# Kernel optimization log

Measured on AMD Instinct MI355X. Metric: run time of the kernel, lower is better.

The kernel has to match this reference:

```python
import jax, jax.numpy as jnp
import numpy as np

# irreps = 128x0e + 64x1e + 32x2e  (dim = 128 + 64*3 + 32*5 = 480)
# hidden = 512x0e + 256x1e + 128x2e ; gate scalars = (256+128) x0e
N = 65536
M0, M1, M2 = 128, 64, 32          # input multiplicities per degree l=0,1,2
H0, H1, H2 = 512, 256, 128        # hidden multiplicities
G = H1 + H2                       # number of sigmoid gate scalars
EPS = 1e-8
S0 = float(np.sqrt(M0)); S1 = float(np.sqrt(M1)); S2 = float(np.sqrt(M2))
T0 = float(np.sqrt(H0)); T1 = float(np.sqrt(H1)); T2 = float(np.sqrt(H2))


def setup_inputs() -> dict:
    key = jax.random.key(0)
    ks = jax.random.split(key, 8)
    p = lambda k, shape: jax.random.normal(k, shape, dtype=jnp.float32)
    return dict(
        x=p(ks[0], (N, M0 + 3 * M1 + 5 * M2)),
        # SeperableLayerNorm affine params (weight per channel; bias only for scalars)
        nw0=jnp.ones((M0,), jnp.float32), nb0=jnp.zeros((M0,), jnp.float32),
        nw1=jnp.ones((M1,), jnp.float32), nw2=jnp.ones((M2,), jnp.float32),
        # lin1: irreps -> (hidden scalars + gates) 0e, hidden 1e, hidden 2e. e3nn fan-in norm.
        W0=p(ks[1], (M0, H0 + G)), b0=jnp.zeros((H0 + G,), jnp.float32),
        W1=p(ks[2], (M1, H1)), W2=p(ks[3], (M2, H2)),
        # lin2: gated hidden -> irreps
        V0=p(ks[4], (H0, M0)), c0=jnp.zeros((M0,), jnp.float32),
        V1=p(ks[5], (H1, M1)), V2=p(ks[6], (H2, M2)),
        alpha=jnp.float32(0.5),
    )


def _ffn(x, nw0, nb0, nw1, nw2, W0, b0, W1, W2, V0, c0, V1, V2, alpha):
    n = x.shape[0]
    x0 = x[:, :M0]                                   # [n, 128] scalars
    x1 = x[:, M0:M0 + 3 * M1].reshape(n, M1, 3)      # [n, 64, 3]
    x2 = x[:, M0 + 3 * M1:].reshape(n, M2, 5)        # [n, 32, 5]

    # --- SeperableLayerNorm (component norm, std_balance_degrees) ---
    # scalars: standard layer norm over scalar channels
    mu = jnp.mean(x0, axis=-1, keepdims=True)
    xc = x0 - mu
    y0 = xc * jax.lax.rsqrt(jnp.mean(xc * xc, axis=-1, keepdims=True) + EPS) * nw0 + nb0
    # l>0: RMS norm, each degree contributes equally (balance over degrees)
    s1 = jnp.mean(x1 * x1, axis=(1, 2))
    s2 = jnp.mean(x2 * x2, axis=(1, 2))
    inv = jax.lax.rsqrt(0.5 * (s1 + s2) + EPS)[:, None, None]
    y1 = x1 * inv * nw1[:, None]
    y2 = x2 * inv * nw2[:, None]

    # --- lin1 (e3nn Linear: per-degree block matmul, 1/sqrt(fan_in), bias on 0e) ---
    h0 = y0 @ W0 / S0 + b0                            # [n, 896]
    h1 = jnp.einsum('num,uw->nwm', y1, W1) / S1       # [n, 256, 3]
    h2 = jnp.einsum('num,uw->nwm', y2, W2) / S2       # [n, 128, 5]

    # --- Gate: silu on hidden scalars, sigmoid gates broadcast onto l>0 ---
    s = jax.nn.silu(h0[:, :H0])
    g = jax.nn.sigmoid(h0[:, H0:])
    z1 = h1 * g[:, :H1, None]
    z2 = h2 * g[:, H1:, None]

    # --- lin2 ---
    o0 = s @ V0 / T0 + c0
    o1 = jnp.einsum('num,uw->nwm', z1, V1) / T1
    o2 = jnp.einsum('num,uw->nwm', z2, V2) / T2
    dx = jnp.concatenate([o0, o1.reshape(n, -1), o2.reshape(n, -1)], axis=-1)
    return x + jnp.tanh(alpha) * dx


def reference(x, nw0, nb0, nw1, nw2, W0, b0, W1, W2, V0, c0, V1, V2, alpha):
    return _ffn(x, nw0, nb0, nw1, nw2, W0, b0, W1, W2, V0, c0, V1, V2, alpha)
```

## Files before the change

### kernel.cpp

```cpp
#include <hip/hip_runtime.h>
#include <stdint.h>

#define NROWS 65536
#define DCOL  480
#define RT    16

#define INV_S0 0.08838834764831845f
#define INV_S1 0.125f
#define INV_S2 0.17677669529663687f
#define INV_T0 0.044194173824159216f
#define INV_T1 0.0625f
#define INV_T2 0.08838834764831845f

#define OFF_W0T 0
#define OFF_W1T 114688
#define OFF_W2T 131072
#define OFF_V0T 135168
#define OFF_V1T 200704
#define OFF_V2T 217088
#define TOT_W   221184

typedef __attribute__((ext_vector_type(8))) short  short8;
typedef __attribute__((ext_vector_type(4))) float  floatx4;

__device__ __forceinline__ uint16_t f2bf(float x){
  uint32_t u = __builtin_bit_cast(uint32_t, x);
  return (uint16_t)((u + 0x8000u) >> 16);
}
__device__ __forceinline__ float bf2f(uint16_t h){
  return __builtin_bit_cast(float, (uint32_t)h << 16);
}

#define MFMA16(a,b,c) __builtin_amdgcn_mfma_f32_16x16x32_bf16((a),(b),(c),0,0,0)

__global__ __launch_bounds__(256)
void convert_weights(const float* __restrict__ W0, const float* __restrict__ W1,
                     const float* __restrict__ W2, const float* __restrict__ V0,
                     const float* __restrict__ V1, const float* __restrict__ V2,
                     uint16_t* __restrict__ wt)
{
  const int tid = blockIdx.x*256 + threadIdx.x;
  if (tid >= TOT_W) return;
  if (tid < OFF_W1T){
    const int i = tid;            const int n = i>>7, k = i&127;
    wt[tid] = f2bf(W0[(size_t)k*896 + n] * INV_S0);
  } else if (tid < OFF_W2T){
    const int i = tid - OFF_W1T;  const int n = i>>6, k = i&63;
    wt[tid] = f2bf(W1[(size_t)k*256 + n] * INV_S1);
  } else if (tid < OFF_V0T){
    const int i = tid - OFF_W2T;  const int n = i>>5, k = i&31;
    wt[tid] = f2bf(W2[(size_t)k*128 + n] * INV_S2);
  } else if (tid < OFF_V1T){
    const int i = tid - OFF_V0T;  const int n = i>>9, k = i&511;
    wt[tid] = f2bf(V0[(size_t)k*128 + n] * INV_T0);
  } else if (tid < OFF_V2T){
    const int i = tid - OFF_V1T;  const int n = i>>8, k = i&255;
    wt[tid] = f2bf(V1[(size_t)k*64 + n] * INV_T1);
  } else {
    const int i = tid - OFF_V2T;  const int n = i>>7, k = i&127;
    wt[tid] = f2bf(V2[(size_t)k*32 + n] * INV_T2);
  }
}

__global__ __launch_bounds__(256, 3)
void ffn_mfma(const float* __restrict__ x,  const float* __restrict__ nw0,
              const float* __restrict__ nb0,const float* __restrict__ nw1,
              const float* __restrict__ nw2,const float* __restrict__ b0,
              const float* __restrict__ c0, const float* __restrict__ alpha,
              const uint16_t* __restrict__ wt, float* __restrict__ out)
{
  __shared__ __align__(16) uint16_t y1bf[3][16][72];
  __shared__ __align__(16) uint16_t y2bf[5][16][40];
  __shared__ __align__(16) uint16_t gbf[16][392];
  __shared__ __align__(16) uint16_t Ubuf[12800];

  uint16_t (*y0bf)[136] = (uint16_t (*)[136])(Ubuf);
  uint16_t (*sbf )[520] = (uint16_t (*)[520])(Ubuf + 2176);
  uint16_t (*z1b0)[264] = (uint16_t (*)[264])(Ubuf + 2176);
  uint16_t (*z1b1)[264] = (uint16_t (*)[264])(Ubuf + 6400);
  uint16_t (*z2b0)[136] = (uint16_t (*)[136])(Ubuf + 10624);
  uint16_t (*z2b1)[136] = (uint16_t (*)[136])(Ubuf);

  const int t      = threadIdx.x;
  const int wave   = t >> 6, lane = t & 63;
  const int lane16 = lane & 15, quad = lane >> 4;
  const int row0   = blockIdx.x * RT;
  const float ta   = tanhf(alpha[0]);
  const floatx4 fz = {0.f,0.f,0.f,0.f};

  {
    float xv[4][8];
    const int rbase = wave*4;
    #pragma unroll
    for (int rr=0; rr<4; ++rr){
      const float* xr = x + (size_t)(row0 + rbase + rr)*DCOL;
      #pragma unroll
      for (int i=0;i<8;++i){ const int e = lane + i*64; xv[rr][i] = (e < DCOL) ? xr[e] : 0.f; }
    }
    float wA[8], wB[8]; int uu[8], mmv[8];
    #pragma unroll
    for (int i=0;i<8;++i){
      const int e = lane + i*64;
      if (e < 128){ uu[i]=e; mmv[i]=0; wA[i]=nw0[e]; wB[i]=nb0[e]; }
      else if (e < 320){ const int d=e-128; const int u=d/3; uu[i]=u; mmv[i]=d-3*u; wA[i]=nw1[u]; wB[i]=0.f; }
      else if (e < DCOL){ const int d=e-320; const int u=d/5; uu[i]=u; mmv[i]=d-5*u; wA[i]=nw2[u]; wB[i]=0.f; }
      else { uu[i]=0; mmv[i]=0; wA[i]=0.f; wB[i]=0.f; }
    }
    #pragma unroll
    for (int rr=0; rr<4; ++rr){
      const int r = rbase + rr;
      float s0  = xv[rr][0] + xv[rr][1];
      float s0q = xv[rr][0]*xv[rr][0] + xv[rr][1]*xv[rr][1];
      float q1  = xv[rr][2]*xv[rr][2] + xv[rr][3]*xv[rr][3] + xv[rr][4]*xv[rr][4];
      float q2  = xv[rr][5]*xv[rr][5] + xv[rr][6]*xv[rr][6] + xv[rr][7]*xv[rr][7];
      #pragma unroll
      for (int off=32; off>0; off>>=1){
        s0  += __shfl_xor(s0,  off);
        s0q += __shfl_xor(s0q, off);
        q1  += __shfl_xor(q1,  off);
        q2  += __shfl_xor(q2,  off);
      }
      const float mu   = s0 * (1.f/128.f);
      const float var  = s0q * (1.f/128.f) - mu*mu;
      const float rstd = rsqrtf(var + 1e-8f);
      const float inv  = rsqrtf(0.5f*(q1*(1.f/192.f) + q2*(1.f/160.f)) + 1e-8f);
      #pragma unroll
      for (int i=0;i<8;++i){
        const int e = lane + i*64;
        if (e < 128)       y0bf[r][e] = f2bf((xv[rr][i]-mu)*rstd*wA[i] + wB[i]);
        else if (e < 320)  y1bf[mmv[i]][r][uu[i]] = f2bf(xv[rr][i]*inv*wA[i]);
        else if (e < DCOL) y2bf[mmv[i]][r][uu[i]] = f2bf(xv[rr][i]*inv*wA[i]);
      }
    }
  }
  __syncthreads();

  {
    short8 a0[4];
    #pragma unroll
    for (int kk=0; kk<4; ++kk)
      a0[kk] = *(const short8*)&y0bf[lane16][kk*32 + quad*8];
    const uint16_t* W0t = wt + OFF_W0T;

    auto ldW0 = [&](int tile, short8* dst){
      #pragma unroll
      for (int kk=0;kk<4;++kk)
        dst[kk] = *(const short8*)(W0t + (size_t)(tile*16+lane16)*128 + kk*32 + quad*8);
    };
    auto h0_tile = [&](int tile, const short8* bfr){
      floatx4 acc = fz;
      #pragma unroll
      for (int kk=0;kk<4;++kk) acc = MFMA16(a0[kk], bfr[kk], acc);
      const int col  = tile*16 + lane16;
      const float bias = b0[col];
      #pragma unroll
      for (int r2=0; r2<4; ++r2){
        const int row = quad*4 + r2;
        const float h  = acc[r2] + bias;
        const float sg = 1.f/(1.f + __expf(-h));
        if (col < 512) sbf[row][col]       = f2bf(h*sg);
        else           gbf[row][col - 512] = f2bf(sg);
      }
    };

    short8 bA[4], bB[4];
    ldW0(wave, bA);
    #pragma unroll 1
    for (int it=0; it<7; ++it){
      const int tA = wave + it*8, tB = tA + 4;
      ldW0(tB, bB);
      h0_tile(tA, bA);
      if (it < 6) ldW0(tA + 8, bA);
      h0_tile(tB, bB);
    }
  }
  __syncthreads();

  {
    const uint16_t* W2t = wt + OFF_W2T;
    const uint16_t* V0t = wt + OFF_V0T;
    const int n0a = wave*16, n0b = (wave+4)*16;
    const short8 a2  = *(const short8*)&y2bf[0][lane16][quad*8];
    const short8 hba = *(const short8*)(W2t + (size_t)(n0a+lane16)*32 + quad*8);
    const short8 hbb = *(const short8*)(W2t + (size_t)(n0b+lane16)*32 + quad*8);
    float xra[4], xrb[4];
    #pragma unroll
    for (int r2=0;r2<4;++r2){
      const int row = quad*4+r2;
      xra[r2] = x[(size_t)(row0+row)*DCOL + n0a + lane16];
      xrb[r2] = x[(size_t)(row0+row)*DCOL + n0b + lane16];
    }
    floatx4 acc0 = fz, acc1 = fz;
    #pragma unroll 4
    for (int kk=0; kk<16; ++kk){
      const short8 a  = *(const short8*)&sbf[lane16][kk*32 + quad*8];
      const short8 ba = *(const short8*)(V0t + (size_t)(n0a+lane16)*512 + kk*32 + quad*8);
      const short8 bb = *(const short8*)(V0t + (size_t)(n0b+lane16)*512 + kk*32 + quad*8);
      acc0 = MFMA16(a, ba, acc0);
      acc1 = MFMA16(a, bb, acc1);
    }
    {
      floatx4 ha = MFMA16(a2, hba, fz);
      floatx4 hb = MFMA16(a2, hbb, fz);
      #pragma unroll
      for (int r2=0;r2<4;++r2){
        const int row = quad*4+r2;
        const int ca = n0a+lane16, cb = n0b+lane16;
        z2b0[row][ca] = f2bf(ha[r2]*bf2f(gbf[row][256+ca]));
        z2b0[row][cb] = f2bf(hb[r2]*bf2f(gbf[row][256+cb]));
      }
    }
    const float cca = c0[n0a+lane16], ccb = c0[n0b+lane16];
    #pragma unroll
    for (int r2=0;r2<4;++r2){
      const int row = quad*4+r2;
      out[(size_t)(row0+row)*DCOL + n0a+lane16] = xra[r2] + ta*(acc0[r2]+cca);
      out[(size_t)(row0+row)*DCOL + n0b+lane16] = xrb[r2] + ta*(acc1[r2]+ccb);
    }
  }
  __syncthreads();

  {
    const uint16_t* W1t = wt + OFF_W1T;
    const uint16_t* W2t = wt + OFF_W2T;
    const uint16_t* V2t = wt + OFF_V2T;
    const int n0a = wave*16, n0b = (wave+4)*16;
    const short8 a2  = *(const short8*)&y2bf[1][lane16][quad*8];
    const short8 hba = *(const short8*)(W2t + (size_t)(n0a+lane16)*32 + quad*8);
    const short8 hbb = *(const short8*)(W2t + (size_t)(n0b+lane16)*32 + quad*8);
    short8 ob[4]; float xro[4];
    if (wave < 2){
      const int n0 = wave*16;
      #pragma unroll
      for (int kk=0;kk<4;++kk)
        ob[kk] = *(const short8*)(V2t + (size_t)(n0+lane16)*128 + kk*32 + quad*8);
      #pragma unroll
      for (int r2=0;r2<4;++r2)
        xro[r2] = x[(size_t)(row0+quad*4+r2)*DCOL + 320 + (n0+lane16)*5 + 0];
    }
    short8 a10[2], a11[2];
    a10[0] = *(const short8*)&y1bf[0][lane16][quad*8];
    a10[1] = *(const short8*)&y1bf[0][lane16][32 + quad*8];
    a11[0] = *(const short8*)&y1bf[1][lane16][quad*8];
    a11[1] = *(const short8*)&y1bf[1][lane16][32 + quad*8];
    #pragma unroll
    for (int t4=0; t4<4; ++t4){
      const int n0 = (wave + t4*4)*16;
      const short8 b0f = *(const short8*)(W1t + (size_t)(n0+lane16)*64 + quad*8);
      const short8 b1f = *(const short8*)(W1t + (size_t)(n0+lane16)*64 + 32 + quad*8);
      floatx4 am0 = fz, am1 = fz;
      am0 = MFMA16(a10[0], b0f, am0); am0 = MFMA16(a10[1], b1f, am0);
      am1 = MFMA16(a11[0], b0f, am1); am1 = MFMA16(a11[1], b1f, am1);
      const int col = n0 + lane16;
      #pragma unroll
      for (int r2=0;r2<4;++r2){
        const int row = quad*4 + r2;
        const float g = bf2f(gbf[row][col]);
        z1b0[row][col] = f2bf(am0[r2]*g);
        z1b1[row][col] = f2bf(am1[r2]*g);
      }
    }
    {
      floatx4 ha = MFMA16(a2, hba, fz);
      floatx4 hb = MFMA16(a2, hbb, fz);
      #pragma unroll
      for (int r2=0;r2<4;++r2){
        const int row = quad*4+r2;
        const int ca = n0a+lane16, cb = n0b+lane16;
        z2b1[row][ca] = f2bf(ha[r2]*bf2f(gbf[row][256+ca]));
        z2b1[row][cb] = f2bf(hb[r2]*bf2f(gbf[row][256+cb]));
      }
    }
    if (wave < 2){
      const int n0 = wave*16;
      floatx4 acc = fz;
      #pragma unroll
      for (int kk=0;kk<4;++kk){
        const short8 a = *(const short8*)&z2b0[lane16][kk*32 + quad*8];
        acc = MFMA16(a, ob[kk], acc);
      }
      const int col = n0 + lane16;
      #pragma unroll
      for (int r2=0;r2<4;++r2){
        const int row = quad*4+r2;
        const size_t idx = (size_t)(row0+row)*DCOL + 320 + col*5 + 0;
        out[idx] = xro[r2] + ta*acc[r2];
      }
    }
  }
  __syncthreads();

  {
    const uint16_t* V1t = wt + OFF_V1T;
    const uint16_t* W2t = wt + OFF_W2T;
    const uint16_t* V2t = wt + OFF_V2T;
    const int n0a = wave*16, n0b = (wave+4)*16;
    const short8 a2  = *(const short8*)&y2bf[2][lane16][quad*8];
    const short8 hba = *(const short8*)(W2t + (size_t)(n0a+lane16)*32 + quad*8);
    const short8 hbb = *(const short8*)(W2t + (size_t)(n0b+lane16)*32 + quad*8);
    short8 ob[4]; float xro[4];
    if (wave >= 2){
      const int n0 = (wave-2)*16;
      #pragma unroll
      for (int kk=0;kk<4;++kk)
        ob[kk] = *(const short8*)(V2t + (size_t)(n0+lane16)*128 + kk*32 + quad*8);
      #pragma unroll
      for (int r2=0;r2<4;++r2)
        xro[r2] = x[(size_t)(row0+quad*4+r2)*DCOL + 320 + (n0+lane16)*5 + 1];
    }
    const int n0 = wave*16;
    float xr0[4], xr1[4];
    #pragma unroll
    for (int r2=0;r2<4;++r2){
      const int row = quad*4+r2;
      xr0[r2] = x[(size_t)(row0+row)*DCOL + 128 + (n0+lane16)*3 + 0];
      xr1[r2] = x[(size_t)(row0+row)*DCOL + 128 + (n0+lane16)*3 + 1];
    }
    floatx4 am0 = fz, am1 = fz;
    #pragma unroll 4
    for (int kk=0; kk<8; ++kk){
      const short8 af0 = *(const short8*)&z1b0[lane16][kk*32 + quad*8];
      const short8 af1 = *(const short8*)&z1b1[lane16][kk*32 + quad*8];
      const short8 b   = *(const short8*)(V1t + (size_t)(n0+lane16)*256 + kk*32 + quad*8);
      am0 = MFMA16(af0, b, am0);
      am1 = MFMA16(af1, b, am1);
    }
    const int col = n0 + lane16;
    #pragma unroll
    for (int r2=0;r2<4;++r2){
      const int row = quad*4+r2;
      out[(size_t)(row0+row)*DCOL + 128 + col*3 + 0] = xr0[r2] + ta*am0[r2];
      out[(size_t)(row0+row)*DCOL + 128 + col*3 + 1] = xr1[r2] + ta*am1[r2];
    }
    {
      floatx4 ha = MFMA16(a2, hba, fz);
      floatx4 hb = MFMA16(a2, hbb, fz);
      #pragma unroll
      for (int r2=0;r2<4;++r2){
        const int row = quad*4+r2;
        const int ca = n0a+lane16, cb = n0b+lane16;
        z2b0[row][ca] = f2bf(ha[r2]*bf2f(gbf[row][256+ca]));
        z2b0[row][cb] = f2bf(hb[r2]*bf2f(gbf[row][256+cb]));
      }
    }
    if (wave >= 2){
      const int n02 = (wave-2)*16;
      floatx4 acc = fz;
      #pragma unroll
      for (int kk=0;kk<4;++kk){
        const short8 a = *(const short8*)&z2b1[lane16][kk*32 + quad*8];
        acc = MFMA16(a, ob[kk], acc);
      }
      const int c2 = n02 + lane16;
      #pragma unroll
      for (int r2=0;r2<4;++r2){
        const int row = quad*4+r2;
        const size_t idx = (size_t)(row0+row)*DCOL + 320 + c2*5 + 1;
        out[idx] = xro[r2] + ta*acc[r2];
      }
    }
  }
  __syncthreads();

  {
    const uint16_t* W1t = wt + OFF_W1T;
    const uint16_t* W2t = wt + OFF_W2T;
    const uint16_t* V2t = wt + OFF_V2T;
    const int n0a = wave*16, n0b = (wave+4)*16;
    const short8 a2  = *(const short8*)&y2bf[3][lane16][quad*8];
    const short8 hba = *(const short8*)(W2t + (size_t)(n0a+lane16)*32 + quad*8);
    const short8 hbb = *(const short8*)(W2t + (size_t)(n0b+lane16)*32 + quad*8);
    short8 ob[4]; float xro[4];
    if (wave < 2){
      const int n0 = wave*16;
      #pragma unroll
      for (int kk=0;kk<4;++kk)
        ob[kk] = *(const short8*)(V2t + (size_t)(n0+lane16)*128 + kk*32 + quad*8);
      #pragma unroll
      for (int r2=0;r2<4;++r2)
        xro[r2] = x[(size_t)(row0+quad*4+r2)*DCOL + 320 + (n0+lane16)*5 + 2];
    }
    short8 a12[2];
    a12[0] = *(const short8*)&y1bf[2][lane16][quad*8];
    a12[1] = *(const short8*)&y1bf[2][lane16][32 + quad*8];
    #pragma unroll
    for (int t4=0; t4<4; ++t4){
      const int n0 = (wave + t4*4)*16;
      const short8 b0f = *(const short8*)(W1t + (size_t)(n0+lane16)*64 + quad*8);
      const short8 b1f = *(const short8*)(W1t + (size_t)(n0+lane16)*64 + 32 + quad*8);
      floatx4 am = fz;
      am = MFMA16(a12[0], b0f, am); am = MFMA16(a12[1], b1f, am);
      const int col = n0 + lane16;
      #pragma unroll
      for (int r2=0;r2<4;++r2){
        const int row = quad*4 + r2;
        z1b0[row][col] = f2bf(am[r2]*bf2f(gbf[row][col]));
      }
    }
    {
      floatx4 ha = MFMA16(a2, hba, fz);
      floatx4 hb = MFMA16(a2, hbb, fz);
      #pragma unroll
      for (int r2=0;r2<4;++r2){
        const int row = quad*4+r2;
        const int ca = n0a+lane16, cb = n0b+lane16;
        z2b1[row][ca] = f2bf(ha[r2]*bf2f(gbf[row][256+ca]));
        z2b1[row][cb] = f2bf(hb[r2]*bf2f(gbf[row][256+cb]));
      }
    }
    if (wave < 2){
      const int n0 = wave*16;
      floatx4 acc = fz;
      #pragma unroll
      for (int kk=0;kk<4;++kk){
        const short8 a = *(const short8*)&z2b0[lane16][kk*32 + quad*8];
        acc = MFMA16(a, ob[kk], acc);
      }
      const int col = n0 + lane16;
      #pragma unroll
      for (int r2=0;r2<4;++r2){
        const int row = quad*4+r2;
        const size_t idx = (size_t)(row0+row)*DCOL + 320 + col*5 + 2;
        out[idx] = xro[r2] + ta*acc[r2];
      }
    }
  }
  __syncthreads();

  {
    const uint16_t* V1t = wt + OFF_V1T;
    const uint16_t* W2t = wt + OFF_W2T;
    const uint16_t* V2t = wt + OFF_V2T;
    const int n0a = wave*16, n0b = (wave+4)*16;
    const short8 a2  = *(const short8*)&y2bf[4][lane16][quad*8];
    const short8 hba = *(const short8*)(W2t + (size_t)(n0a+lane16)*32 + quad*8);
    const short8 hbb = *(const short8*)(W2t + (size_t)(n0b+lane16)*32 + quad*8);
    short8 ob[4]; float xro[4];
    if (wave >= 2){
      const int n0 = (wave-2)*16;
      #pragma unroll
      for (int kk=0;kk<4;++kk)
        ob[kk] = *(const short8*)(V2t + (size_t)(n0+lane16)*128 + kk*32 + quad*8);
      #pragma unroll
      for (int r2=0;r2<4;++r2)
        xro[r2] = x[(size_t)(row0+quad*4+r2)*DCOL + 320 + (n0+lane16)*5 + 3];
    }
    const int n0 = wave*16;
    float xr2[4];
    #pragma unroll
    for (int r2=0;r2<4;++r2)
      xr2[r2] = x[(size_t)(row0+quad*4+r2)*DCOL + 128 + (n0+lane16)*3 + 2];
    floatx4 am = fz;
    #pragma unroll 4
    for (int kk=0; kk<8; ++kk){
      const short8 a = *(const short8*)&z1b0[lane16][kk*32 + quad*8];
      const short8 b = *(const short8*)(V1t + (size_t)(n0+lane16)*256 + kk*32 + quad*8);
      am = MFMA16(a, b, am);
    }
    const int col = n0 + lane16;
    #pragma unroll
    for (int r2=0;r2<4;++r2){
      const int row = quad*4+r2;
      out[(size_t)(row0+row)*DCOL + 128 + col*3 + 2] = xr2[r2] + ta*am[r2];
    }
    {
      floatx4 ha = MFMA16(a2, hba, fz);
      floatx4 hb = MFMA16(a2, hbb, fz);
      #pragma unroll
      for (int r2=0;r2<4;++r2){
        const int row = quad*4+r2;
        const int ca = n0a+lane16, cb = n0b+lane16;
        z2b0[row][ca] = f2bf(ha[r2]*bf2f(gbf[row][256+ca]));
        z2b0[row][cb] = f2bf(hb[r2]*bf2f(gbf[row][256+cb]));
      }
    }
    if (wave >= 2){
      const int n02 = (wave-2)*16;
      floatx4 acc = fz;
      #pragma unroll
      for (int kk=0;kk<4;++kk){
        const short8 a = *(const short8*)&z2b1[lane16][kk*32 + quad*8];
        acc = MFMA16(a, ob[kk], acc);
      }
      const int c2 = n02 + lane16;
      #pragma unroll
      for (int r2=0;r2<4;++r2){
        const int row = quad*4+r2;
        const size_t idx = (size_t)(row0+row)*DCOL + 320 + c2*5 + 3;
        out[idx] = xro[r2] + ta*acc[r2];
      }
    }
  }
  __syncthreads();

  if (wave < 2){
    const uint16_t* V2t = wt + OFF_V2T;
    const int n0 = wave*16;
    short8 ob[4]; float xro[4];
    #pragma unroll
    for (int kk=0;kk<4;++kk)
      ob[kk] = *(const short8*)(V2t + (size_t)(n0+lane16)*128 + kk*32 + quad*8);
    #pragma unroll
    for (int r2=0;r2<4;++r2)
      xro[r2] = x[(size_t)(row0+quad*4+r2)*DCOL + 320 + (n0+lane16)*5 + 4];
    floatx4 acc = fz;
    #pragma unroll
    for (int kk=0;kk<4;++kk){
      const short8 a = *(const short8*)&z2b0[lane16][kk*32 + quad*8];
      acc = MFMA16(a, ob[kk], acc);
    }
    const int col = n0 + lane16;
    #pragma unroll
    for (int r2=0;r2<4;++r2){
      const int row = quad*4+r2;
      const size_t idx = (size_t)(row0+row)*DCOL + 320 + col*5 + 4;
      out[idx] = xro[r2] + ta*acc[r2];
    }
  }
}

extern "C" void kernel_launch(void* const* d_in, const int* in_sizes, int n_in,
                              void* d_out, int out_size, void* d_ws, size_t ws_size,
                              hipStream_t stream) {
  const float* x   = (const float*)d_in[0];
  const float* nw0 = (const float*)d_in[1];
  const float* nb0 = (const float*)d_in[2];
  const float* nw1 = (const float*)d_in[3];
  const float* nw2 = (const float*)d_in[4];
  const float* W0  = (const float*)d_in[5];
  const float* b0  = (const float*)d_in[6];
  const float* W1  = (const float*)d_in[7];
  const float* W2  = (const float*)d_in[8];
  const float* V0  = (const float*)d_in[9];
  const float* c0  = (const float*)d_in[10];
  const float* V1  = (const float*)d_in[11];
  const float* V2  = (const float*)d_in[12];
  const float* al  = (const float*)d_in[13];
  uint16_t* wt = (uint16_t*)d_ws;

  convert_weights<<<dim3((TOT_W + 255)/256), dim3(256), 0, stream>>>(
      W0, W1, W2, V0, V1, V2, wt);
  ffn_mfma<<<dim3(NROWS/RT), dim3(256), 0, stream>>>(
      x, nw0, nb0, nw1, nw2, b0, c0, al, wt, (float*)d_out);
}
```

Baseline: 471.4 us.

## Double waves per block to 8 and redistribute per-stage tile work

Launches 512 threads per 16-row block instead of 256, halving each wave's share of the work. Each wave now handles one output tile per stage, and the LN, h0, l=1 and l=2 stages are reassigned across the eight waves. The aim is more latency hiding and more parallel MFMA issue within each block. In exchange it raises the per-block thread count and the register-pressure target, and leaves some waves idle in the smaller stages.

```diff
diff --git a/kernel.cpp b/kernel.cpp
--- a/kernel.cpp
+++ b/kernel.cpp
@@ -62,7 +62,7 @@
   }
 }
 
-__global__ __launch_bounds__(256, 3)
+__global__ __launch_bounds__(512, 6)
 void ffn_mfma(const float* __restrict__ x,  const float* __restrict__ nw0,
               const float* __restrict__ nb0,const float* __restrict__ nw1,
               const float* __restrict__ nw2,const float* __restrict__ b0,
@@ -89,10 +89,10 @@
   const floatx4 fz = {0.f,0.f,0.f,0.f};
 
   {
-    float xv[4][8];
-    const int rbase = wave*4;
-    #pragma unroll
-    for (int rr=0; rr<4; ++rr){
+    float xv[2][8];
+    const int rbase = wave*2;
+    #pragma unroll
+    for (int rr=0; rr<2; ++rr){
       const float* xr = x + (size_t)(row0 + rbase + rr)*DCOL;
       #pragma unroll
       for (int i=0;i<8;++i){ const int e = lane + i*64; xv[rr][i] = (e < DCOL) ? xr[e] : 0.f; }
@@ -107,7 +107,7 @@
       else { uu[i]=0; mmv[i]=0; wA[i]=0.f; wB[i]=0.f; }
     }
     #pragma unroll
-    for (int rr=0; rr<4; ++rr){
+    for (int rr=0; rr<2; ++rr){
       const int r = rbase + rr;
       float s0  = xv[rr][0] + xv[rr][1];
       float s0q = xv[rr][0]*xv[rr][0] + xv[rr][1]*xv[rr][1];
@@ -163,15 +163,13 @@
       }
     };
 
-    short8 bA[4], bB[4];
-    ldW0(wave, bA);
-    #pragma unroll 1
+    short8 buf[2][4];
+    ldW0(wave, buf[0]);
+    #pragma unroll
     for (int it=0; it<7; ++it){
-      const int tA = wave + it*8, tB = tA + 4;
-      ldW0(tB, bB);
-      h0_tile(tA, bA);
-      if (it < 6) ldW0(tA + 8, bA);
-      h0_tile(tB, bB);
+      const int cur = it & 1;
+      if (it < 6) ldW0(wave + (it+1)*8, buf[cur^1]);
+      h0_tile(wave + it*8, buf[cur]);
     }
   }
   __syncthreads();
@@ -179,43 +177,34 @@
   {
     const uint16_t* W2t = wt + OFF_W2T;
     const uint16_t* V0t = wt + OFF_V0T;
-    const int n0a = wave*16, n0b = (wave+4)*16;
-    const short8 a2  = *(const short8*)&y2bf[0][lane16][quad*8];
-    const short8 hba = *(const short8*)(W2t + (size_t)(n0a+lane16)*32 + quad*8);
-    const short8 hbb = *(const short8*)(W2t + (size_t)(n0b+lane16)*32 + quad*8);
-    float xra[4], xrb[4];
-    #pragma unroll
-    for (int r2=0;r2<4;++r2){
-      const int row = quad*4+r2;
-      xra[r2] = x[(size_t)(row0+row)*DCOL + n0a + lane16];
-      xrb[r2] = x[(size_t)(row0+row)*DCOL + n0b + lane16];
-    }
-    floatx4 acc0 = fz, acc1 = fz;
+    const int n0 = wave*16;
+    const int col = n0 + lane16;
+    const short8 a2 = *(const short8*)&y2bf[0][lane16][quad*8];
+    const short8 hb = *(const short8*)(W2t + (size_t)col*32 + quad*8);
+    float xra[4];
+    #pragma unroll
+    for (int r2=0;r2<4;++r2)
+      xra[r2] = x[(size_t)(row0+quad*4+r2)*DCOL + col];
+    floatx4 acc0 = fz;
     #pragma unroll 4
     for (int kk=0; kk<16; ++kk){
       const short8 a  = *(const short8*)&sbf[lane16][kk*32 + quad*8];
-      const short8 ba = *(const short8*)(V0t + (size_t)(n0a+lane16)*512 + kk*32 + quad*8);
-      const short8 bb = *(const short8*)(V0t + (size_t)(n0b+lane16)*512 + kk*32 + quad*8);
+      const short8 ba = *(const short8*)(V0t + (size_t)col*512 + kk*32 + quad*8);
       acc0 = MFMA16(a, ba, acc0);
-      acc1 = MFMA16(a, bb, acc1);
     }
     {
-      floatx4 ha = MFMA16(a2, hba, fz);
-      floatx4 hb = MFMA16(a2, hbb, fz);
-      #pragma unroll
-      for (int r2=0;r2<4;++r2){
-        const int row = quad*4+r2;
-        const int ca = n0a+lane16, cb = n0b+lane16;
-        z2b0[row][ca] = f2bf(ha[r2]*bf2f(gbf[row][256+ca]));
-        z2b0[row][cb] = f2bf(hb[r2]*bf2f(gbf[row][256+cb]));
-      }
-    }
-    const float cca = c0[n0a+lane16], ccb = c0[n0b+lane16];
+      floatx4 ha = MFMA16(a2, hb, fz);
+      #pragma unroll
+      for (int r2=0;r2<4;++r2){
+        const int row = quad*4+r2;
+        z2b0[row][col] = f2bf(ha[r2]*bf2f(gbf[row][256+col]));
+      }
+    }
+    const float cca = c0[col];
     #pragma unroll
     for (int r2=0;r2<4;++r2){
       const int row = quad*4+r2;
-      out[(size_t)(row0+row)*DCOL + n0a+lane16] = xra[r2] + ta*(acc0[r2]+cca);
-      out[(size_t)(row0+row)*DCOL + n0b+lane16] = xrb[r2] + ta*(acc1[r2]+ccb);
+      out[(size_t)(row0+row)*DCOL + col] = xra[r2] + ta*(acc0[r2]+cca);
     }
   }
   __syncthreads();
@@ -224,10 +213,9 @@
     const uint16_t* W1t = wt + OFF_W1T;
     const uint16_t* W2t = wt + OFF_W2T;
     const uint16_t* V2t = wt + OFF_V2T;
-    const int n0a = wave*16, n0b = (wave+4)*16;
-    const short8 a2  = *(const short8*)&y2bf[1][lane16][quad*8];
-    const short8 hba = *(const short8*)(W2t + (size_t)(n0a+lane16)*32 + quad*8);
-    const short8 hbb = *(const short8*)(W2t + (size_t)(n0b+lane16)*32 + quad*8);
+    const int hcol = wave*16 + lane16;
+    const short8 a2 = *(const short8*)&y2bf[1][lane16][quad*8];
+    const short8 hb = *(const short8*)(W2t + (size_t)hcol*32 + quad*8);
     short8 ob[4]; float xro[4];
     if (wave < 2){
       const int n0 = wave*16;
@@ -244,8 +232,8 @@
     a11[0] = *(const short8*)&y1bf[1][lane16][quad*8];
     a11[1] = *(const short8*)&y1bf[1][lane16][32 + quad*8];
     #pragma unroll
-    for (int t4=0; t4<4; ++t4){
-      const int n0 = (wave + t4*4)*16;
+    for (int tt=0; tt<2; ++tt){
+      const int n0 = (wave + tt*8)*16;
       const short8 b0f = *(const short8*)(W1t + (size_t)(n0+lane16)*64 + quad*8);
       const short8 b1f = *(const short8*)(W1t + (size_t)(n0+lane16)*64 + 32 + quad*8);
       floatx4 am0 = fz, am1 = fz;
@@ -261,14 +249,11 @@
       }
     }
     {
-      floatx4 ha = MFMA16(a2, hba, fz);
-      floatx4 hb = MFMA16(a2, hbb, fz);
-      #pragma unroll
-      for (int r2=0;r2<4;++r2){
-        const int row = quad*4+r2;
-        const int ca = n0a+lane16, cb = n0b+lane16;
-        z2b1[row][ca] = f2bf(ha[r2]*bf2f(gbf[row][256+ca]));
-        z2b1[row][cb] = f2bf(hb[r2]*bf2f(gbf[row][256+cb]));
+      floatx4 ha = MFMA16(a2, hb, fz);
+      #pragma unroll
+      for (int r2=0;r2<4;++r2){
+        const int row = quad*4+r2;
+        z2b1[row][hcol] = f2bf(ha[r2]*bf2f(gbf[row][256+hcol]));
       }
     }
     if (wave < 2){
@@ -294,12 +279,11 @@
     const uint16_t* V1t = wt + OFF_V1T;
     const uint16_t* W2t = wt + OFF_W2T;
     const uint16_t* V2t = wt + OFF_V2T;
-    const int n0a = wave*16, n0b = (wave+4)*16;
-    const short8 a2  = *(const short8*)&y2bf[2][lane16][quad*8];
-    const short8 hba = *(const short8*)(W2t + (size_t)(n0a+lane16)*32 + quad*8);
-    const short8 hbb = *(const short8*)(W2t + (size_t)(n0b+lane16)*32 + quad*8);
+    const int hcol = wave*16 + lane16;
+    const short8 a2 = *(const short8*)&y2bf[2][lane16][quad*8];
+    const short8 hb = *(const short8*)(W2t + (size_t)hcol*32 + quad*8);
     short8 ob[4]; float xro[4];
-    if (wave >= 2){
+    if (wave == 2 || wave == 3){
       const int n0 = (wave-2)*16;
       #pragma unroll
       for (int kk=0;kk<4;++kk)
@@ -308,42 +292,35 @@
       for (int r2=0;r2<4;++r2)
         xro[r2] = x[(size_t)(row0+quad*4+r2)*DCOL + 320 + (n0+lane16)*5 + 1];
     }
-    const int n0 = wave*16;
-    float xr0[4], xr1[4];
+    const int mo = wave >> 2;
+    const int n0 = (wave & 3)*16;
+    const int col = n0 + lane16;
+    float xr0[4];
+    #pragma unroll
+    for (int r2=0;r2<4;++r2)
+      xr0[r2] = x[(size_t)(row0+quad*4+r2)*DCOL + 128 + col*3 + mo];
+    const uint16_t (*zb)[264] = mo ? z1b1 : z1b0;
+    floatx4 am0 = fz;
+    #pragma unroll 4
+    for (int kk=0; kk<8; ++kk){
+      const short8 af = *(const short8*)&zb[lane16][kk*32 + quad*8];
+      const short8 b  = *(const short8*)(V1t + (size_t)col*256 + kk*32 + quad*8);
+      am0 = MFMA16(af, b, am0);
+    }
     #pragma unroll
     for (int r2=0;r2<4;++r2){
       const int row = quad*4+r2;
-      xr0[r2] = x[(size_t)(row0+row)*DCOL + 128 + (n0+lane16)*3 + 0];
-      xr1[r2] = x[(size_t)(row0+row)*DCOL + 128 + (n0+lane16)*3 + 1];
-    }
-    floatx4 am0 = fz, am1 = fz;
-    #pragma unroll 4
-    for (int kk=0; kk<8; ++kk){
-      const short8 af0 = *(const short8*)&z1b0[lane16][kk*32 + quad*8];
-      const short8 af1 = *(const short8*)&z1b1[lane16][kk*32 + quad*8];
-      const short8 b   = *(const short8*)(V1t + (size_t)(n0+lane16)*256 + kk*32 + quad*8);
-      am0 = MFMA16(af0, b, am0);
-      am1 = MFMA16(af1, b, am1);
-    }
-    const int col = n0 + lane16;
-    #pragma unroll
-    for (int r2=0;r2<4;++r2){
-      const int row = quad*4+r2;
-      out[(size_t)(row0+row)*DCOL + 128 + col*3 + 0] = xr0[r2] + ta*am0[r2];
-      out[(size_t)(row0+row)*DCOL + 128 + col*3 + 1] = xr1[r2] + ta*am1[r2];
+      out[(size_t)(row0+row)*DCOL + 128 + col*3 + mo] = xr0[r2] + ta*am0[r2];
     }
     {
-      floatx4 ha = MFMA16(a2, hba, fz);
-      floatx4 hb = MFMA16(a2, hbb, fz);
-      #pragma unroll
-      for (int r2=0;r2<4;++r2){
-        const int row = quad*4+r2;
-        const int ca = n0a+lane16, cb = n0b+lane16;
-        z2b0[row][ca] = f2bf(ha[r2]*bf2f(gbf[row][256+ca]));
-        z2b0[row][cb] = f2bf(hb[r2]*bf2f(gbf[row][256+cb]));
-      }
-    }
-    if (wave >= 2){
+      floatx4 ha = MFMA16(a2, hb, fz);
+      #pragma unroll
+      for (int r2=0;r2<4;++r2){
+        const int row = quad*4+r2;
+        z2b0[row][hcol] = f2bf(ha[r2]*bf2f(gbf[row][256+hcol]));
+      }
+    }
+    if (wave == 2 || wave == 3){
       const int n02 = (wave-2)*16;
       floatx4 acc = fz;
       #pragma unroll
@@ -366,13 +343,12 @@
     const uint16_t* W1t = wt + OFF_W1T;
     const uint16_t* W2t = wt + OFF_W2T;
     const uint16_t* V2t = wt + OFF_V2T;
-    const int n0a = wave*16, n0b = (wave+4)*16;
-    const short8 a2  = *(const short8*)&y2bf[3][lane16][quad*8];
-    const short8 hba = *(const short8*)(W2t + (size_t)(n0a+lane16)*32 + quad*8);
-    const short8 hbb = *(const short8*)(W2t + (size_t)(n0b+lane16)*32 + quad*8);
+    const int hcol = wave*16 + lane16;
+    const short8 a2 = *(const short8*)&y2bf[3][lane16][quad*8];
+    const short8 hb = *(const short8*)(W2t + (size_t)hcol*32 + quad*8);
     short8 ob[4]; float xro[4];
-    if (wave < 2){
-      const int n0 = wave*16;
+    if (wave == 4 || wave == 5){
+      const int n0 = (wave-4)*16;
       #pragma unroll
       for (int kk=0;kk<4;++kk)
         ob[kk] = *(const short8*)(V2t + (size_t)(n0+lane16)*128 + kk*32 + quad*8);
@@ -384,8 +360,8 @@
     a12[0] = *(const short8*)&y1bf[2][lane16][quad*8];
     a12[1] = *(const short8*)&y1bf[2][lane16][32 + quad*8];
     #pragma unroll
-    for (int t4=0; t4<4; ++t4){
-      const int n0 = (wave + t4*4)*16;
+    for (int tt=0; tt<2; ++tt){
+      const int n0 = (wave + tt*8)*16;
       const short8 b0f = *(const short8*)(W1t + (size_t)(n0+lane16)*64 + quad*8);
       const short8 b1f = *(const short8*)(W1t + (size_t)(n0+lane16)*64 + 32 + quad*8);
       floatx4 am = fz;
@@ -398,18 +374,15 @@
       }
     }
     {
-      floatx4 ha = MFMA16(a2, hba, fz);
-      floatx4 hb = MFMA16(a2, hbb, fz);
-      #pragma unroll
-      for (int r2=0;r2<4;++r2){
-        const int row = quad*4+r2;
-        const int ca = n0a+lane16, cb = n0b+lane16;
-        z2b1[row][ca] = f2bf(ha[r2]*bf2f(gbf[row][256+ca]));
-        z2b1[row][cb] = f2bf(hb[r2]*bf2f(gbf[row][256+cb]));
-      }
-    }
-    if (wave < 2){
-      const int n0 = wave*16;
+      floatx4 ha = MFMA16(a2, hb, fz);
+      #pragma unroll
+      for (int r2=0;r2<4;++r2){
+        const int row = quad*4+r2;
+        z2b1[row][hcol] = f2bf(ha[r2]*bf2f(gbf[row][256+hcol]));
+      }
+    }
+    if (wave == 4 || wave == 5){
+      const int n0 = (wave-4)*16;
       floatx4 acc = fz;
       #pragma unroll
       for (int kk=0;kk<4;++kk){
@@ -431,13 +404,12 @@
     const uint16_t* V1t = wt + OFF_V1T;
     const uint16_t* W2t = wt + OFF_W2T;
     const uint16_t* V2t = wt + OFF_V2T;
-    const int n0a = wave*16, n0b = (wave+4)*16;
-    const short8 a2  = *(const short8*)&y2bf[4][lane16][quad*8];
-    const short8 hba = *(const short8*)(W2t + (size_t)(n0a+lane16)*32 + quad*8);
-    const short8 hbb = *(const short8*)(W2t + (size_t)(n0b+lane16)*32 + quad*8);
+    const int hcol = wave*16 + lane16;
+    const short8 a2 = *(const short8*)&y2bf[4][lane16][quad*8];
+    const short8 hb = *(const short8*)(W2t + (size_t)hcol*32 + quad*8);
     short8 ob[4]; float xro[4];
-    if (wave >= 2){
-      const int n0 = (wave-2)*16;
+    if (wave >= 6){
+      const int n0 = (wave-6)*16;
       #pragma unroll
       for (int kk=0;kk<4;++kk)
         ob[kk] = *(const short8*)(V2t + (size_t)(n0+lane16)*128 + kk*32 + quad*8);
@@ -445,37 +417,36 @@
       for (int r2=0;r2<4;++r2)
         xro[r2] = x[(size_t)(row0+quad*4+r2)*DCOL + 320 + (n0+lane16)*5 + 3];
     }
-    const int n0 = wave*16;
-    float xr2[4];
-    #pragma unroll
-    for (int r2=0;r2<4;++r2)
-      xr2[r2] = x[(size_t)(row0+quad*4+r2)*DCOL + 128 + (n0+lane16)*3 + 2];
-    floatx4 am = fz;
-    #pragma unroll 4
-    for (int kk=0; kk<8; ++kk){
-      const short8 a = *(const short8*)&z1b0[lane16][kk*32 + quad*8];
-      const short8 b = *(const short8*)(V1t + (size_t)(n0+lane16)*256 + kk*32 + quad*8);
-      am = MFMA16(a, b, am);
-    }
-    const int col = n0 + lane16;
-    #pragma unroll
-    for (int r2=0;r2<4;++r2){
-      const int row = quad*4+r2;
-      out[(size_t)(row0+row)*DCOL + 128 + col*3 + 2] = xr2[r2] + ta*am[r2];
+    if (wave < 4){
+      const int n0 = wave*16;
+      const int col = n0 + lane16;
+      float xr2[4];
+      #pragma unroll
+      for (int r2=0;r2<4;++r2)
+        xr2[r2] = x[(size_t)(row0+quad*4+r2)*DCOL + 128 + col*3 + 2];
+      floatx4 am = fz;
+      #pragma unroll 4
+      for (int kk=0; kk<8; ++kk){
+        const short8 a = *(const short8*)&z1b0[lane16][kk*32 + quad*8];
+        const short8 b = *(const short8*)(V1t + (size_t)col*256 + kk*32 + quad*8);
+        am = MFMA16(a, b, am);
+      }
+      #pragma unroll
+      for (int r2=0;r2<4;++r2){
+        const int row = quad*4+r2;
+        out[(size_t)(row0+row)*DCOL + 128 + col*3 + 2] = xr2[r2] + ta*am[r2];
+      }
     }
     {
-      floatx4 ha = MFMA16(a2, hba, fz);
-      floatx4 hb = MFMA16(a2, hbb, fz);
-      #pragma unroll
-      for (int r2=0;r2<4;++r2){
-        const int row = quad*4+r2;
-        const int ca = n0a+lane16, cb = n0b+lane16;
-        z2b0[row][ca] = f2bf(ha[r2]*bf2f(gbf[row][256+ca]));
-        z2b0[row][cb] = f2bf(hb[r2]*bf2f(gbf[row][256+cb]));
-      }
-    }
-    if (wave >= 2){
-      const int n02 = (wave-2)*16;
+      floatx4 ha = MFMA16(a2, hb, fz);
+      #pragma unroll
+      for (int r2=0;r2<4;++r2){
+        const int row = quad*4+r2;
+        z2b0[row][hcol] = f2bf(ha[r2]*bf2f(gbf[row][256+hcol]));
+      }
+    }
+    if (wave >= 6){
+      const int n02 = (wave-6)*16;
       floatx4 acc = fz;
       #pragma unroll
       for (int kk=0;kk<4;++kk){
@@ -540,6 +511,6 @@
 
   convert_weights<<<dim3((TOT_W + 255)/256), dim3(256), 0, stream>>>(
       W0, W1, W2, V0, V1, V2, wt);
-  ffn_mfma<<<dim3(NROWS/RT), dim3(256), 0, stream>>>(
+  ffn_mfma<<<dim3(NROWS/RT), dim3(512), 0, stream>>>(
       x, nw0, nb0, nw1, nw2, b0, c0, al, wt, (float*)d_out);
 }
```

Result: slower. 530.6 us (+12.6%).
